# Kernel optimization log

Measured on AMD Instinct MI355X. Metric: run time of the kernel, lower is better.

## Reference

```python
import jax, jax.numpy as jnp
import numpy as np


def setup_inputs() -> dict:
    key = jax.random.key(0)
    ks = jax.random.split(key, 8)
    batch, seqlen, nheads, headdim = 2, 2048, 64, 64
    ngroups, dstate = 1, 128
    x = jax.random.normal(ks[0], (batch, seqlen, nheads, headdim), jnp.float32)
    dt = jax.random.uniform(ks[1], (batch, seqlen, nheads), jnp.float32)
    # A must be negative for a stable decaying SSM
    A = -jax.random.uniform(ks[2], (nheads,), jnp.float32, minval=1.0, maxval=8.0)
    B = jax.random.normal(ks[3], (batch, seqlen, ngroups, dstate), jnp.float32)
    C = jax.random.normal(ks[4], (batch, seqlen, ngroups, dstate), jnp.float32)
    D = jax.random.uniform(ks[5], (nheads,), jnp.float32)
    z = jax.random.normal(ks[6], (batch, seqlen, nheads, headdim), jnp.float32)
    dt_bias = jax.random.uniform(ks[7], (nheads,), jnp.float32)
    return {"x": x, "dt": dt, "A": A, "B": B, "C": C, "D": D, "z": z,
            "dt_bias": dt_bias, "chunk_size": 256}


def _ssd_chunk_scan_combined(x, dt, A, B, C, D, z, dt_bias, chunk_size):
    batch, seqlen, nheads, headdim = x.shape
    ngroups, dstate = B.shape[2], B.shape[3]
    nchunks = seqlen // chunk_size  # seqlen chosen divisible by chunk_size

    # dt: (b, l, h) -> (b, h, c, s); bias + softplus, fp32
    dt = dt.astype(jnp.float32).reshape(batch, nchunks, chunk_size, nheads).transpose(0, 3, 1, 2)
    dt = jax.nn.softplus(dt + dt_bias.astype(jnp.float32)[None, :, None, None])
    dA = dt * A.astype(jnp.float32)[None, :, None, None]        # (b,h,c,s)
    dA_cumsum = jnp.cumsum(dA, axis=-1)                          # (b,h,c,s)

    # broadcast B/C groups to heads: 'b l g n -> b l (g h) n'
    rep = nheads // ngroups
    Bc = jnp.repeat(B, rep, axis=2).reshape(batch, nchunks, chunk_size, nheads, dstate)
    Cc = jnp.repeat(C, rep, axis=2).reshape(batch, nchunks, chunk_size, nheads, dstate)
    xc = x.reshape(batch, nchunks, chunk_size, nheads, headdim)

    # ---- chunk_state: per-chunk end-state contributions ----
    decay_states = jnp.exp(dA_cumsum[..., -1:] - dA_cumsum)      # (b,h,c,s)
    states = jnp.einsum('bcshn,bhcs,bcshp->bchpn', Bc, decay_states * dt, xc)

    # ---- state_passing: propagate states across chunks ----
    dA_last = dA_cumsum[..., -1]                                 # (b,h,c)
    csum = jnp.cumsum(jnp.pad(dA_last, ((0, 0), (0, 0), (1, 0))), axis=-1)  # (b,h,c+1)
    seg = csum[:, :, :, None] - csum[:, :, None, :]
    cmask = jnp.tril(jnp.ones((nchunks + 1, nchunks + 1), bool))
    decay_chunk = jnp.where(cmask, jnp.exp(seg), 0.0)            # (b,h,c+1,c+1)
    states_flat = states.reshape(batch, nchunks, nheads, headdim * dstate)
    states_cat = jnp.concatenate([jnp.zeros_like(states_flat[:, :1]), states_flat], axis=1)
    outs = jnp.einsum('bhzc,bchd->bzhd', decay_chunk, states_cat)
    prev_states = outs[:, :-1].reshape(batch, nchunks, nheads, headdim, dstate)
    final_states = outs[:, -1].reshape(batch, nheads, headdim, dstate)

    # ---- chunk_scan: intra-chunk attention-like scan + inter-chunk term ----
    CB = jnp.einsum('bclhn,bcshn->bchls', Cc, Bc)                # (b,c,h,l,s)
    decay = jnp.exp(dA_cumsum[:, :, :, :, None] - dA_cumsum[:, :, :, None, :])  # (b,h,c,l,s)
    scores = CB * decay.transpose(0, 2, 1, 3, 4)                 # (b,c,h,l,s)
    tri = jnp.tril(jnp.ones((chunk_size, chunk_size), bool))
    scores = jnp.where(tri, scores, 0.0)
    out = jnp.einsum('bchls,bhcs,bcshp->bclhp', scores, dt, xc)
    state_decay_out = jnp.exp(dA_cumsum).transpose(0, 2, 3, 1)[..., None]       # (b,c,l,h,1)
    out = out + jnp.einsum('bclhn,bchpn->bclhp', Cc, prev_states) * state_decay_out
    out = out.reshape(batch, seqlen, nheads, headdim)

    out = out + x * D[None, None, :, None]
    out = out * jax.nn.silu(z)
    return out.astype(x.dtype), final_states


def reference(x, dt, A, B, C, D, z, dt_bias, chunk_size):
    return _ssd_chunk_scan_combined(x, dt, A, B, C, D, z, dt_bias, chunk_size)
```

## Files before the change

### kernel.cpp

```cpp
#include <hip/hip_runtime.h>
#include <math.h>

#define BATCH 2
#define SEQ   2048
#define NH    64
#define HD    64
#define DS    128
#define CS    256
#define NC    8
#define LOG2E 1.4426950408889634f

typedef __attribute__((ext_vector_type(8))) short s16x8;
typedef __attribute__((ext_vector_type(4))) float f32x4;

#define MFMA16(a,b,c) __builtin_amdgcn_mfma_f32_16x16x32_bf16(a, b, c, 0, 0, 0)

__device__ inline unsigned cvt_pk_bf16(float a, float b) {
    unsigned r;
    asm("v_cvt_pk_bf16_f32 %0, %1, %2" : "=v"(r) : "v"(a), "v"(b));
    return r;
}
__device__ inline float exp2f_fast(float x) {
#if __has_builtin(__builtin_amdgcn_exp2f)
    return __builtin_amdgcn_exp2f(x);
#else
    float r;
    asm("v_exp_f32 %0, %1" : "=v"(r) : "v"(x));
    return r;
#endif
}
__device__ inline float2 unpack2bf(unsigned u) {
    return make_float2(__uint_as_float(u << 16), __uint_as_float(u & 0xffff0000u));
}

union frag_u { unsigned u[4]; s16x8 v; };

__global__ __launch_bounds__(CS) void k1_dt(
    const float* __restrict__ dt, const float* __restrict__ A,
    const float* __restrict__ dt_bias,
    float* __restrict__ dtp, float* __restrict__ dacs)
{
    int bid = blockIdx.x;
    int c = bid % NC;
    int h = (bid / NC) % NH;
    int b = bid / (NC * NH);
    int s = threadIdx.x;

    float v  = dt[((size_t)b * SEQ + c * CS + s) * NH + h] + dt_bias[h];
    float sp = fmaxf(v, 0.f) + log1pf(__expf(-fabsf(v)));
    float dA = sp * (A[h] * LOG2E);

    __shared__ float sm[CS];
    sm[s] = dA;
    __syncthreads();
    for (int off = 1; off < CS; off <<= 1) {
        float tt = (s >= off) ? sm[s - off] : 0.f;
        __syncthreads();
        sm[s] += tt;
        __syncthreads();
    }
    size_t o = (size_t)bid * CS + s;
    dtp[o]  = sp;
    dacs[o] = sm[s];
}

__global__ __launch_bounds__(256) void k0a_xdt(
    const float* __restrict__ x, const float* __restrict__ dtp,
    unsigned* __restrict__ xdt)
{
    int bid = blockIdx.x;
    int h = bid & 63, c = (bid >> 6) & 7, b = bid >> 9;
    int t = threadIdx.x;
    size_t dt_base = ((size_t)(b*NH + h)*NC + c)*CS;
    __shared__ float tile[64][65];
    __shared__ float dtS[64];
    for (int st = 0; st < 4; ++st) {
        int s0 = st * 64;
        __syncthreads();
        if (t < 64) dtS[t] = dtp[dt_base + s0 + t];
        #pragma unroll
        for (int i = 0; i < 16; ++i) {
            int f = t + i * 256;
            int row = f >> 6, col = f & 63;
            tile[row][col] = x[((size_t)(b*SEQ + c*CS + s0 + row)*NH + h)*HD + col];
        }
        __syncthreads();
        #pragma unroll
        for (int i = 0; i < 8; ++i) {
            int f = t + i * 256;
            int p = f >> 5, sd = f & 31;
            xdt[((size_t)bid*64 + p)*128 + (s0 >> 1) + sd] =
                cvt_pk_bf16(tile[2*sd][p] * dtS[2*sd], tile[2*sd+1][p] * dtS[2*sd+1]);
        }
    }
}

__global__ __launch_bounds__(256) void k0b_cast(
    const float* __restrict__ src, unsigned* __restrict__ dst)
{
    size_t f = (size_t)blockIdx.x * 256 + threadIdx.x;
    const float4* s4 = (const float4*)(src + f * 8);
    float4 a = s4[0], bq = s4[1];
    uint4 o;
    o.x = cvt_pk_bf16(a.x,  a.y);  o.y = cvt_pk_bf16(a.z,  a.w);
    o.z = cvt_pk_bf16(bq.x, bq.y); o.w = cvt_pk_bf16(bq.z, bq.w);
    *(uint4*)(dst + f * 4) = o;
}

__global__ __launch_bounds__(256) void k0c_BT(
    const float* __restrict__ Bg, unsigned* __restrict__ BT)
{
    int bid = blockIdx.x;
    int st = bid & 3, nt = (bid >> 2) & 1, bc = bid >> 3;
    int b = bc >> 3, c = bc & 7;
    int s0 = st * 64, n0 = nt * 64;
    int t = threadIdx.x;
    __shared__ float tile[64][65];
    #pragma unroll
    for (int i = 0; i < 16; ++i) {
        int f = t + i * 256;
        int row = f >> 6, col = f & 63;
        tile[row][col] = Bg[(size_t)(b*SEQ + c*CS + s0 + row)*DS + n0 + col];
    }
    __syncthreads();
    #pragma unroll
    for (int i = 0; i < 8; ++i) {
        int f = t + i * 256;
        int n = f >> 5, sd = f & 31;
        BT[((size_t)bc*128 + n0 + n)*128 + (s0 >> 1) + sd] =
            cvt_pk_bf16(tile[2*sd][n], tile[2*sd+1][n]);
    }
}

__global__ __launch_bounds__(256) void k2_cb(
    const float* __restrict__ Bg_, const float* __restrict__ Cg_,
    unsigned* __restrict__ cb_bf)
{
    const int TLt[10] = {0,1,1,2,2,2,3,3,3,3};
    const int TSt[10] = {0,0,1,0,1,2,0,1,2,3};
    int bid = blockIdx.x;
    int ti = bid % 10;
    int bc = bid / 10;
    int tl = TLt[ti], ts = TSt[ti];
    int b = bc / NC, c = bc % NC;

    const float* Cg = Cg_ + (size_t)(b * SEQ + c * CS + tl * 64) * DS;
    const float* Bg = Bg_ + (size_t)(b * SEQ + c * CS + ts * 64) * DS;

    __shared__ __align__(16) float Ct[32][68];
    __shared__ __align__(16) float Bt[32][68];

    int t  = threadIdx.x;
    int tx = t & 15, ty = t >> 4;
    int s0 = tx * 4, l0 = ty * 4;
    float acc[4][4] = {};

    for (int n0 = 0; n0 < DS; n0 += 32) {
        __syncthreads();
        {
            int r  = t >> 5;
            int nn = t & 31;
            #pragma unroll
            for (int i = 0; i < 8; ++i) {
                Ct[nn][r + i * 8] = Cg[(size_t)(r + i * 8) * DS + n0 + nn];
                Bt[nn][r + i * 8] = Bg[(size_t)(r + i * 8) * DS + n0 + nn];
            }
        }
        __syncthreads();
        #pragma unroll 8
        for (int n = 0; n < 32; ++n) {
            float4 cv = *(const float4*)&Ct[n][l0];
            float4 bv = *(const float4*)&Bt[n][s0];
            float cva[4] = {cv.x, cv.y, cv.z, cv.w};
            float bva[4] = {bv.x, bv.y, bv.z, bv.w};
            #pragma unroll
            for (int i = 0; i < 4; ++i)
                #pragma unroll
                for (int j = 0; j < 4; ++j)
                    acc[i][j] += cva[i] * bva[j];
        }
    }

    unsigned* cbg = cb_bf + (size_t)bc * 32768;
    #pragma unroll
    for (int i = 0; i < 4; ++i) {
        int row  = tl * 64 + l0 + i;
        int colb = (ts * 64 + s0) >> 1;
        uint2 wv;
        wv.x = cvt_pk_bf16(acc[i][0], acc[i][1]);
        wv.y = cvt_pk_bf16(acc[i][2], acc[i][3]);
        *(uint2*)&cbg[(size_t)row * 128 + colb] = wv;
    }
}

__global__ __launch_bounds__(256) void k3_chunk_state(
    const unsigned* __restrict__ xdt, const unsigned* __restrict__ BT,
    const float* __restrict__ dacs, unsigned short* __restrict__ states_bf)
{
    int bid = blockIdx.x;
    int bc = bid >> 6;
    int h = bid & 63, c = (bid >> 6) & 7, b = bid >> 9;
    int t = threadIdx.x;
    int w = t >> 6, lane = t & 63, m16 = lane & 15, q = lane >> 4;

    size_t dt_base = ((size_t)(b*NH + h)*NC + c)*CS;
    __shared__ float coS[CS];
    {
        float daL = dacs[dt_base + CS - 1];
        coS[t] = exp2f_fast(daL - dacs[dt_base + t]);
    }
    __syncthreads();

    const unsigned* xb = xdt + (size_t)bid * 8192;
    const unsigned* bb = BT + (size_t)bc * 16384;

    f32x4 acc[8] = {};

    #pragma unroll
    for (int ks = 0; ks < 4; ++ks) {
        #pragma unroll
        for (int kk = 0; kk < 2; ++kk) {
            int kd = ks*32 + kk*16 + q*4;
            int sbase = ks*64 + kk*32 + q*8;
            uint4 xq = *(const uint4*)&xb[(w*16 + m16)*128 + kd];
            float co8[8];
            *(float4*)&co8[0] = *(const float4*)&coS[sbase];
            *(float4*)&co8[4] = *(const float4*)&coS[sbase + 4];
            frag_u af;
            {
                float2 v0 = unpack2bf(xq.x), v1 = unpack2bf(xq.y);
                float2 v2 = unpack2bf(xq.z), v3 = unpack2bf(xq.w);
                af.u[0] = cvt_pk_bf16(v0.x*co8[0], v0.y*co8[1]);
                af.u[1] = cvt_pk_bf16(v1.x*co8[2], v1.y*co8[3]);
                af.u[2] = cvt_pk_bf16(v2.x*co8[4], v2.y*co8[5]);
                af.u[3] = cvt_pk_bf16(v3.x*co8[6], v3.y*co8[7]);
            }
            #pragma unroll
            for (int nt = 0; nt < 8; ++nt) {
                s16x8 bf8 = *(const s16x8*)&bb[(nt*16 + m16)*128 + kd];
                acc[nt] = MFMA16(af.v, bf8, acc[nt]);
            }
        }
    }

    unsigned short* sg = states_bf + (size_t)bid * 8192;
    #pragma unroll
    for (int nt = 0; nt < 8; ++nt) {
        #pragma unroll
        for (int r = 0; r < 4; r += 2) {
            int p = w*16 + q*4 + r;
            unsigned u = cvt_pk_bf16(acc[nt][r], acc[nt][r+1]);
            sg[p*128 + nt*16 + m16]     = (unsigned short)u;
            sg[(p+1)*128 + nt*16 + m16] = (unsigned short)(u >> 16);
        }
    }
}

__global__ __launch_bounds__(256) void k4_state_passing(
    const unsigned* __restrict__ states_bf, const float* __restrict__ dacs,
    unsigned* __restrict__ prevT, float* __restrict__ final_states)
{
    int e = blockIdx.x * 256 + threadIdx.x;
    int n2 = e & 63;
    int p  = (e >> 6) & 63;
    int h  = (e >> 12) & 63;
    int b  = e >> 18;

    float r0 = 0.f, r1 = 0.f;
    #pragma unroll
    for (int c = 0; c < NC; ++c) {
        size_t idx = (((size_t)(b*NC + c)*NH + h)*HD + p)*64 + n2;
        float2 vv = unpack2bf(states_bf[idx]);
        prevT[idx] = cvt_pk_bf16(r0, r1);
        float el = exp2f_fast(dacs[((size_t)(b*NH + h)*NC + c)*CS + CS - 1]);
        r0 = el * r0 + vv.x;
        r1 = el * r1 + vv.y;
    }
    float* fg = final_states + (((size_t)(b*NH + h)*HD + p)*DS + 2*n2);
    fg[0] = r0; fg[1] = r1;
}

__global__ __launch_bounds__(256) void k5_chunk_scan(
    const float* __restrict__ x, const float* __restrict__ z,
    const unsigned* __restrict__ Cb, const float* __restrict__ Dp,
    const float* __restrict__ dacs, const unsigned* __restrict__ cb_bf,
    const unsigned* __restrict__ xdt, const unsigned* __restrict__ prevT,
    float* __restrict__ out)
{
    int bid = blockIdx.x;
    int h = bid & 63, c = (bid >> 6) & 7, b = bid >> 9;
    int bc = bid >> 6;
    int t = threadIdx.x;
    int w = t >> 6, lane = t & 63, m16 = lane & 15, q = lane >> 4;

    __shared__ float dacsS[CS];
    __shared__ float elS[CS];
    size_t dt_base = ((size_t)(b*NH + h)*NC + c)*CS;
    {
        float dv = dacs[dt_base + t];
        dacsS[t] = dv;
        elS[t]   = exp2f_fast(dv);
    }
    __syncthreads();

    const unsigned* xb  = xdt + (size_t)bid * 8192;
    const unsigned* cbb = cb_bf + (size_t)bc * 32768;

    f32x4 acc[4][4] = {};
    float dlv[4];
    #pragma unroll
    for (int jj = 0; jj < 4; ++jj) dlv[jj] = dacsS[(w + 4*jj)*16 + m16];

    #pragma unroll
    for (int st = 0; st < 4; ++st) {
        int s0 = st * 64;
        #pragma unroll
        for (int kk = 0; kk < 2; ++kk) {
            int kd = (s0 >> 1) + kk*16 + q*4;
            s16x8 bfr[4];
            #pragma unroll
            for (int pt = 0; pt < 4; ++pt)
                bfr[pt] = *(const s16x8*)&xb[(pt*16 + m16)*128 + kd];
            int sbase = s0 + kk*32 + q*8;
            float ds8[8];
            *(float4*)&ds8[0] = *(const float4*)&dacsS[sbase];
            *(float4*)&ds8[4] = *(const float4*)&dacsS[sbase + 4];
            #pragma unroll
            for (int jj = st; jj < 4; ++jj) {
                if (st == jj && kk == 1 && w == 0) continue;
                int lrow = (w + 4*jj)*16 + m16;
                float dl = dlv[jj];
                uint4 cbq = *(const uint4*)&cbb[(size_t)lrow*128 + kd];
                frag_u af;
                float2 v0 = unpack2bf(cbq.x), v1 = unpack2bf(cbq.y);
                float2 v2 = unpack2bf(cbq.z), v3 = unpack2bf(cbq.w);
                float wv[8];
                wv[0] = v0.x * exp2f_fast(dl - ds8[0]);
                wv[1] = v0.y * exp2f_fast(dl - ds8[1]);
                wv[2] = v1.x * exp2f_fast(dl - ds8[2]);
                wv[3] = v1.y * exp2f_fast(dl - ds8[3]);
                wv[4] = v2.x * exp2f_fast(dl - ds8[4]);
                wv[5] = v2.y * exp2f_fast(dl - ds8[5]);
                wv[6] = v3.x * exp2f_fast(dl - ds8[6]);
                wv[7] = v3.y * exp2f_fast(dl - ds8[7]);
                if (st == jj) {
                    #pragma unroll
                    for (int j = 0; j < 8; ++j)
                        wv[j] = (sbase + j <= lrow) ? wv[j] : 0.f;
                }
                af.u[0] = cvt_pk_bf16(wv[0], wv[1]);
                af.u[1] = cvt_pk_bf16(wv[2], wv[3]);
                af.u[2] = cvt_pk_bf16(wv[4], wv[5]);
                af.u[3] = cvt_pk_bf16(wv[6], wv[7]);
                #pragma unroll
                for (int pt = 0; pt < 4; ++pt)
                    acc[jj][pt] = MFMA16(af.v, bfr[pt], acc[jj][pt]);
            }
        }
    }

    {
        const unsigned* pb = prevT + (size_t)bid * 4096;
        float elv[4];
        #pragma unroll
        for (int jj = 0; jj < 4; ++jj) elv[jj] = elS[(w + 4*jj)*16 + m16];
        #pragma unroll
        for (int kq = 0; kq < 4; ++kq) {
            int kd = kq*16 + q*4;
            s16x8 pfr[4];
            #pragma unroll
            for (int pt = 0; pt < 4; ++pt)
                pfr[pt] = *(const s16x8*)&pb[(pt*16 + m16)*64 + kd];
            #pragma unroll
            for (int jj = 0; jj < 4; ++jj) {
                int lrow = (w + 4*jj)*16 + m16;
                uint4 cq = *(const uint4*)&Cb[(size_t)(b*SEQ + c*CS + lrow)*64 + kd];
                float el = elv[jj];
                frag_u af;
                float2 v0 = unpack2bf(cq.x), v1 = unpack2bf(cq.y);
                float2 v2 = unpack2bf(cq.z), v3 = unpack2bf(cq.w);
                af.u[0] = cvt_pk_bf16(v0.x*el, v0.y*el);
                af.u[1] = cvt_pk_bf16(v1.x*el, v1.y*el);
                af.u[2] = cvt_pk_bf16(v2.x*el, v2.y*el);
                af.u[3] = cvt_pk_bf16(v3.x*el, v3.y*el);
                #pragma unroll
                for (int pt = 0; pt < 4; ++pt)
                    acc[jj][pt] = MFMA16(af.v, pfr[pt], acc[jj][pt]);
            }
        }
    }

    float Dh = Dp[h];
    #pragma unroll
    for (int jj = 0; jj < 4; ++jj) {
        #pragma unroll
        for (int r = 0; r < 4; ++r) {
            int l = (w + 4*jj)*16 + q*4 + r;
            size_t gro = ((size_t)(b*SEQ + c*CS + l)*NH + h)*HD;
            #pragma unroll
            for (int pt = 0; pt < 4; ++pt) {
                int p = pt*16 + m16;
                float xv = x[gro + p], zv = z[gro + p];
                float o = acc[jj][pt][r] + xv * Dh;
                float sig = 1.f / (1.f + __expf(-zv));
                out[gro + p] = o * (zv * sig);
            }
        }
    }
}

extern "C" void kernel_launch(void* const* d_in, const int* in_sizes, int n_in,
                              void* d_out, int out_size, void* d_ws, size_t ws_size,
                              hipStream_t stream)
{
    (void)in_sizes; (void)n_in; (void)out_size; (void)ws_size;
    const float* x       = (const float*)d_in[0];
    const float* dt      = (const float*)d_in[1];
    const float* A       = (const float*)d_in[2];
    const float* B       = (const float*)d_in[3];
    const float* C       = (const float*)d_in[4];
    const float* D       = (const float*)d_in[5];
    const float* z       = (const float*)d_in[6];
    const float* dt_bias = (const float*)d_in[7];

    float* out           = (float*)d_out;
    float* final_states  = out + (size_t)BATCH * SEQ * NH * HD;

    float* ws        = (float*)d_ws;
    float* dtp       = ws;
    float* dacs      = dtp + 262144;
    unsigned short* states_bf = (unsigned short*)(dacs + 262144);
    unsigned* prevT  = (unsigned*)(states_bf + 8388608);
    unsigned* cb_bf  = prevT + 4194304;
    unsigned* xdt    = cb_bf + 524288;
    unsigned* BT     = xdt + 8388608;
    unsigned* Cb     = BT + 262144;

    k1_dt   <<<BATCH * NH * NC, CS,  0, stream>>>(dt, A, dt_bias, dtp, dacs);
    k0a_xdt <<<BATCH * NC * NH, 256, 0, stream>>>(x, dtp, xdt);
    k0b_cast<<<256,             256, 0, stream>>>(C, Cb);
    k0c_BT  <<<BATCH * NC * 8,  256, 0, stream>>>(B, BT);
    k2_cb   <<<BATCH * NC * 10, 256, 0, stream>>>(B, C, cb_bf);
    k3_chunk_state<<<BATCH * NC * NH, 256, 0, stream>>>(xdt, BT, dacs, states_bf);
    k4_state_passing<<<(BATCH * NH * HD * DS / 2) / 256, 256, 0, stream>>>(
        (const unsigned*)states_bf, dacs, prevT, final_states);
    k5_chunk_scan<<<BATCH * NC * NH, 256, 0, stream>>>(x, z, Cb, D, dacs,
                                                       cb_bf, xdt, prevT, out);
}
```

Before: 327.0 us.

## Stage xdt tile in swizzled LDS and vectorize epilogue via LDS transpose

```diff
diff --git a/kernel.cpp b/kernel.cpp
--- a/kernel.cpp
+++ b/kernel.cpp
@@ -280,7 +280,7 @@
     fg[0] = r0; fg[1] = r1;
 }
 
-__global__ __launch_bounds__(256) void k5_chunk_scan(
+__global__ __launch_bounds__(256, 4) void k5_chunk_scan(
     const float* __restrict__ x, const float* __restrict__ z,
     const unsigned* __restrict__ Cb, const float* __restrict__ Dp,
     const float* __restrict__ dacs, const unsigned* __restrict__ cb_bf,
@@ -293,9 +293,19 @@
     int t = threadIdx.x;
     int w = t >> 6, lane = t & 63, m16 = lane & 15, q = lane >> 4;
 
+    __shared__ __align__(16) unsigned xbL[8192];
     __shared__ float dacsS[CS];
     __shared__ float elS[CS];
     size_t dt_base = ((size_t)(b*NH + h)*NC + c)*CS;
+    const unsigned* xb  = xdt + (size_t)bid * 8192;
+
+    #pragma unroll
+    for (int ps = 0; ps < 8; ++ps) {
+        int d = ps*1024 + t*4;
+        uint4 v = *(const uint4*)&xb[d];
+        unsigned ba = ((unsigned)d << 2) ^ ((((unsigned)d >> 7) & 7u) << 4);
+        *(uint4*)((char*)xbL + ba) = v;
+    }
     {
         float dv = dacs[dt_base + t];
         dacsS[t] = dv;
@@ -303,13 +313,14 @@
     }
     __syncthreads();
 
-    const unsigned* xb  = xdt + (size_t)bid * 8192;
     const unsigned* cbb = cb_bf + (size_t)bc * 32768;
 
     f32x4 acc[4][4] = {};
     float dlv[4];
     #pragma unroll
     for (int jj = 0; jj < 4; ++jj) dlv[jj] = dacsS[(w + 4*jj)*16 + m16];
+
+    int rsw = (m16 & 7) << 4;
 
     #pragma unroll
     for (int st = 0; st < 4; ++st) {
@@ -319,8 +330,10 @@
             int kd = (s0 >> 1) + kk*16 + q*4;
             s16x8 bfr[4];
             #pragma unroll
-            for (int pt = 0; pt < 4; ++pt)
-                bfr[pt] = *(const s16x8*)&xb[(pt*16 + m16)*128 + kd];
+            for (int pt = 0; pt < 4; ++pt) {
+                unsigned ba = ((unsigned)((pt*16 + m16)*128 + kd) << 2) ^ rsw;
+                bfr[pt] = *(const s16x8*)((const char*)xbL + ba);
+            }
             int sbase = s0 + kk*32 + q*8;
             float ds8[8];
             *(float4*)&ds8[0] = *(const float4*)&dacsS[sbase];
@@ -391,20 +404,34 @@
     }
 
     float Dh = Dp[h];
-    #pragma unroll
-    for (int jj = 0; jj < 4; ++jj) {
+    float* tb = (float*)xbL;
+    int lr_r = t >> 2;
+    int qd   = t & 3;
+    #pragma unroll
+    for (int g = 0; g < 4; ++g) {
+        __syncthreads();
         #pragma unroll
         for (int r = 0; r < 4; ++r) {
-            int l = (w + 4*jj)*16 + q*4 + r;
-            size_t gro = ((size_t)(b*SEQ + c*CS + l)*NH + h)*HD;
-            #pragma unroll
-            for (int pt = 0; pt < 4; ++pt) {
-                int p = pt*16 + m16;
-                float xv = x[gro + p], zv = z[gro + p];
-                float o = acc[jj][pt][r] + xv * Dh;
-                float sig = 1.f / (1.f + __expf(-zv));
-                out[gro + p] = o * (zv * sig);
-            }
+            int lr = w*16 + q*4 + r;
+            #pragma unroll
+            for (int pt = 0; pt < 4; ++pt)
+                tb[lr*68 + pt*16 + m16] = acc[g][pt][r];
+        }
+        __syncthreads();
+        int l = g*64 + lr_r;
+        size_t gro = ((size_t)(b*SEQ + c*CS + l)*NH + h)*HD;
+        #pragma unroll
+        for (int i = 0; i < 4; ++i) {
+            int f4 = qd + 4*i;
+            float4 av = *(const float4*)&tb[lr_r*68 + f4*4];
+            float4 xv = *(const float4*)&x[gro + f4*4];
+            float4 zv = *(const float4*)&z[gro + f4*4];
+            float4 ov;
+            ov.x = (av.x + xv.x*Dh) * (zv.x / (1.f + __expf(-zv.x)));
+            ov.y = (av.y + xv.y*Dh) * (zv.y / (1.f + __expf(-zv.y)));
+            ov.z = (av.z + xv.z*Dh) * (zv.z / (1.f + __expf(-zv.z)));
+            ov.w = (av.w + xv.w*Dh) * (zv.w / (1.f + __expf(-zv.w)));
+            *(float4*)&out[gro + f4*4] = ov;
         }
     }
 }
```

Measured after the change: 333.1 us. Within noise of the previous version (+1.9%).
